# Kernel optimization log

Hardware: AMD Instinct MI355X
Metric: run time of the kernel (lower is better)

The kernel has to match this reference:

```python
import jax, jax.numpy as jnp
import numpy as np

B, IN_DIM, HID = 4096, 1024, 1024


def _linear(x, W, b):
    # torch nn.Linear: y = x @ W.T + b, W is [out, in]
    return x @ W.T + b


def setup_inputs() -> dict:
    key = jax.random.key(0)
    ks = jax.random.split(key, 15)
    s_in = 1.0 / np.sqrt(IN_DIM + HID)
    s_x = 1.0 / np.sqrt(IN_DIM)
    s_h = 1.0 / np.sqrt(HID)
    return {
        "x": jax.random.normal(ks[0], (B, IN_DIM), jnp.float32),
        "h_prev": jax.random.normal(ks[1], (B, HID), jnp.float32),
        "c_prev": jax.random.normal(ks[2], (B, HID), jnp.float32),
        "Wi": jax.random.normal(ks[3], (HID, IN_DIM + HID), jnp.float32) * s_in,
        "bi": jax.random.normal(ks[4], (HID,), jnp.float32) * s_in,
        "Wf": jax.random.normal(ks[5], (HID, IN_DIM + HID), jnp.float32) * s_in,
        "bf": jax.random.normal(ks[6], (HID,), jnp.float32) * s_in,
        "Wo": jax.random.normal(ks[7], (HID, IN_DIM + HID), jnp.float32) * s_in,
        "bo": jax.random.normal(ks[8], (HID,), jnp.float32) * s_in,
        "Wxs": jax.random.normal(ks[9], (HID, IN_DIM), jnp.float32) * s_x,
        "bxs": jax.random.normal(ks[10], (HID,), jnp.float32) * s_x,
        "Wxg": jax.random.normal(ks[11], (HID, IN_DIM), jnp.float32) * s_x,
        "bxg": jax.random.normal(ks[12], (HID,), jnp.float32) * s_x,
        "Whg": jax.random.normal(ks[13], (HID, HID), jnp.float32) * s_h,
        "bhg": jax.random.normal(ks[14], (HID,), jnp.float32) * s_h,
    }


def reference(x, h_prev, c_prev, Wi, bi, Wf, bf, Wo, bo, Wxs, bxs, Wxg, bxg, Whg, bhg):
    # Fuse the three (in_dim+hid)->hid gate GEMMs into one concatenated GEMM.
    concat = jnp.concatenate([x, h_prev], axis=-1)          # [B, in_dim+hid]
    W_ifo = jnp.concatenate([Wi, Wf, Wo], axis=0)           # [3*hid, in_dim+hid]
    b_ifo = jnp.concatenate([bi, bf, bo], axis=0)           # [3*hid]
    gates = jax.nn.sigmoid(_linear(concat, W_ifo, b_ifo))   # [B, 3*hid]
    i_t, f_t, o_t = jnp.split(gates, 3, axis=-1)
    s_t = _linear(x, Wxs, bxs)
    cand_lin = _linear(x, Wxg, bxg) + _linear(h_prev, Whg, bhg)
    g_t = jnp.tanh(s_t * cand_lin)
    # refined=False branch
    c_t = f_t * c_prev + i_t * g_t
    h_t = o_t * jnp.tanh(c_t)
    return (h_t, c_t)
```

## Files before the change

kernel.cpp:

```cpp
#include <hip/hip_runtime.h>

typedef unsigned short u16;
typedef __attribute__((ext_vector_type(8))) __bf16 bf16x8;
typedef __attribute__((ext_vector_type(4))) float f32x4;
typedef __attribute__((ext_vector_type(4))) unsigned short u16x4;

#define AS1 __attribute__((address_space(1)))
#define AS3 __attribute__((address_space(3)))

#define OB_X    0L
#define OB_H    4194304L
#define OB_WI   8388608L
#define OB_WF   10485760L
#define OB_WO   12582912L
#define OB_WXS  14680064L
#define OB_WXG  15728640L
#define OB_WHG  16777216L
#define BLOB_EL 17825792L
#define BLOB_BYTES (BLOB_EL * 2)

__device__ __forceinline__ float b2f(u16 u) {
    return __uint_as_float(((unsigned)u) << 16);
}
__device__ __forceinline__ u16 f2b(float f) {
    unsigned u = __float_as_uint(f);
    u += 0x7fffu + ((u >> 16) & 1u);
    return (u16)(u >> 16);
}
__device__ __forceinline__ f32x4 loadY4(const u16* p) {
    u16x4 v = *(const u16x4*)p;
    f32x4 r;
    r.x = b2f(v.x); r.y = b2f(v.y); r.z = b2f(v.z); r.w = b2f(v.w);
    return r;
}

__global__ __launch_bounds__(256) void convert_all(
    const float* __restrict__ x, const float* __restrict__ h,
    const float* __restrict__ Wi, const float* __restrict__ Wf,
    const float* __restrict__ Wo, const float* __restrict__ Wxs,
    const float* __restrict__ Wxg, const float* __restrict__ Whg,
    u16* __restrict__ blob)
{
    long e = ((long)blockIdx.x * 256 + threadIdx.x) * 8;
    const float* src; long off;
    if      (e < OB_H)   { src = x;   off = e; }
    else if (e < OB_WI)  { src = h;   off = e - OB_H; }
    else if (e < OB_WF)  { src = Wi;  off = e - OB_WI; }
    else if (e < OB_WO)  { src = Wf;  off = e - OB_WF; }
    else if (e < OB_WXS) { src = Wo;  off = e - OB_WO; }
    else if (e < OB_WXG) { src = Wxs; off = e - OB_WXS; }
    else if (e < OB_WHG) { src = Wxg; off = e - OB_WXG; }
    else                 { src = Whg; off = e - OB_WHG; }
    f32x4 v0 = *(const f32x4*)(src + off);
    f32x4 v1 = *(const f32x4*)(src + off + 4);
    u16x4 o0, o1;
    o0.x = f2b(v0.x); o0.y = f2b(v0.y); o0.z = f2b(v0.z); o0.w = f2b(v0.w);
    o1.x = f2b(v1.x); o1.y = f2b(v1.y); o1.z = f2b(v1.z); o1.w = f2b(v1.w);
    *(u16x4*)(blob + e) = o0;
    *(u16x4*)(blob + e + 4) = o1;
}

__global__ __launch_bounds__(256, 3) void srulstm_gemm(
    const u16* __restrict__ blob, u16* __restrict__ Y)
{
    __shared__ __align__(16) u16 As[128 * 64];
    __shared__ __align__(16) u16 Bs[128 * 64];

    const u16* x   = blob + OB_X;
    const u16* h   = blob + OB_H;
    const u16* Wi  = blob + OB_WI;
    const u16* Wf  = blob + OB_WF;
    const u16* Wo  = blob + OB_WO;
    const u16* Wxs = blob + OB_WXS;
    const u16* Wxg = blob + OB_WXG;
    const u16* Whg = blob + OB_WHG;

    const int t = threadIdx.x;
    const int n0 = blockIdx.x * 128;
    const int m0 = blockIdx.y * 128;
    const int seg = n0 >> 10;
    const int row0 = n0 & 1023;

    const u16* bLo; const u16* bHi; int bLd; int kLim;
    if (seg == 0)      { bLo = Wi  + row0 * 2048; bHi = bLo + 1024;        bLd = 2048; kLim = 2048; }
    else if (seg == 1) { bLo = Wf  + row0 * 2048; bHi = bLo + 1024;        bLd = 2048; kLim = 2048; }
    else if (seg == 2) { bLo = Wo  + row0 * 2048; bHi = bLo + 1024;        bLd = 2048; kLim = 2048; }
    else if (seg == 3) { bLo = Wxg + row0 * 1024; bHi = Whg + row0 * 1024; bLd = 1024; kLim = 2048; }
    else               { bLo = Wxs + row0 * 1024; bHi = bLo;               bLd = 1024; kLim = 1024; }

    const u16* aLo = x + m0 * 1024;
    const u16* aHi = h + m0 * 1024;

    const int lane = t & 63;
    const int wave = t >> 6;
    const int wm = (wave >> 1) << 6;
    const int wn = (wave & 1) << 6;
    const int fr = lane & 15;
    const int fq = lane >> 4;
    const int r7 = fr & 7;

    f32x4 acc[4][4] = {};

    const int er = t >> 3;
    const int gsw = (((t & 7) ^ (er & 7)) << 3);

    for (int k0 = 0; k0 < kLim; k0 += 64) {
        const int kc = k0 & 1023;
        const u16* aSrc = ((k0 < 1024) ? aLo : aHi) + kc;
        const u16* bSrc = ((k0 < 1024) ? bLo : bHi) + kc;
#pragma unroll
        for (int it = 0; it < 4; ++it) {
            const int row = it * 32 + er;
            __builtin_amdgcn_global_load_lds(
                (AS1 void*)(aSrc + row * 1024 + gsw),
                (AS3 void*)(As + (it * 256 + t) * 8), 16, 0, 0);
        }
#pragma unroll
        for (int it = 0; it < 4; ++it) {
            const int row = it * 32 + er;
            __builtin_amdgcn_global_load_lds(
                (AS1 void*)(bSrc + row * bLd + gsw),
                (AS3 void*)(Bs + (it * 256 + t) * 8), 16, 0, 0);
        }
        __syncthreads();
#pragma unroll
        for (int kk = 0; kk < 64; kk += 32) {
            const int sw = ((((kk >> 3) + fq) ^ r7) << 3);
            bf16x8 a[4], b[4];
#pragma unroll
            for (int mi = 0; mi < 4; ++mi)
                a[mi] = *(const bf16x8*)(As + (wm + mi * 16 + fr) * 64 + sw);
#pragma unroll
            for (int ni = 0; ni < 4; ++ni)
                b[ni] = *(const bf16x8*)(Bs + (wn + ni * 16 + fr) * 64 + sw);
#pragma unroll
            for (int mi = 0; mi < 4; ++mi)
#pragma unroll
                for (int ni = 0; ni < 4; ++ni)
                    acc[mi][ni] = __builtin_amdgcn_mfma_f32_16x16x32_bf16(
                        a[mi], b[ni], acc[mi][ni], 0, 0, 0);
        }
        __syncthreads();
    }

    const int orow = m0 + wm + (fq << 2);
    const int ocol = n0 + wn + fr;
#pragma unroll
    for (int mi = 0; mi < 4; ++mi)
#pragma unroll
        for (int ni = 0; ni < 4; ++ni) {
            u16* yp = Y + (long)(orow + mi * 16) * 5120 + (ocol + ni * 16);
#pragma unroll
            for (int r = 0; r < 4; ++r)
                yp[(long)r * 5120] = f2b(acc[mi][ni][r]);
        }
}

__global__ __launch_bounds__(256) void srulstm_epilogue(
    const u16* __restrict__ Y, const float* __restrict__ c_prev,
    const float* __restrict__ bi, const float* __restrict__ bfv,
    const float* __restrict__ bo, const float* __restrict__ bxs,
    const float* __restrict__ bxg, const float* __restrict__ bhg,
    float* __restrict__ out)
{
    const int gid = blockIdx.x * 256 + threadIdx.x;
    const int b = gid >> 8;
    const int j = (gid & 255) << 2;
    const long yb = (long)b * 5120 + j;

    f32x4 zi = loadY4(Y + yb);
    f32x4 zf = loadY4(Y + yb + 1024);
    f32x4 zo = loadY4(Y + yb + 2048);
    f32x4 zc = loadY4(Y + yb + 3072);
    f32x4 zs = loadY4(Y + yb + 4096);

    f32x4 cp  = *(const f32x4*)(c_prev + (long)b * 1024 + j);
    f32x4 vbi = *(const f32x4*)(bi + j);
    f32x4 vbf = *(const f32x4*)(bfv + j);
    f32x4 vbo = *(const f32x4*)(bo + j);
    f32x4 vbs = *(const f32x4*)(bxs + j);
    f32x4 vbg = *(const f32x4*)(bxg + j);
    f32x4 vbh = *(const f32x4*)(bhg + j);

    f32x4 ho, co;
#pragma unroll
    for (int r = 0; r < 4; ++r) {
        float i_t = 1.f / (1.f + __expf(-(zi[r] + vbi[r])));
        float f_t = 1.f / (1.f + __expf(-(zf[r] + vbf[r])));
        float o_t = 1.f / (1.f + __expf(-(zo[r] + vbo[r])));
        float s_t = zs[r] + vbs[r];
        float cand = zc[r] + vbg[r] + vbh[r];
        float g_t = tanhf(s_t * cand);
        float c_t = f_t * cp[r] + i_t * g_t;
        float h_t = o_t * tanhf(c_t);
        ho[r] = h_t;
        co[r] = c_t;
    }
    *(f32x4*)(out + (long)b * 1024 + j) = ho;
    *(f32x4*)(out + 4194304L + (long)b * 1024 + j) = co;
}

extern "C" void kernel_launch(void* const* d_in, const int* in_sizes, int n_in,
                              void* d_out, int out_size, void* d_ws, size_t ws_size,
                              hipStream_t stream)
{
    u16* blob = (u16*)d_ws;
    u16* Y = blob + BLOB_EL;
    float* out = (float*)d_out;

    dim3 gg(40, 32), gb(256);
    dim3 eg(4096), eb(256);
    const long convBlocks = BLOB_EL / 8 / 256;

    convert_all<<<dim3(convBlocks), dim3(256), 0, stream>>>(
        (const float*)d_in[0], (const float*)d_in[1], (const float*)d_in[3],
        (const float*)d_in[5], (const float*)d_in[7], (const float*)d_in[9],
        (const float*)d_in[11], (const float*)d_in[13], blob);

    srulstm_gemm<<<gg, gb, 0, stream>>>(blob, Y);

    srulstm_epilogue<<<eg, eb, 0, stream>>>(
        Y, (const float*)d_in[2], (const float*)d_in[4], (const float*)d_in[6],
        (const float*)d_in[8], (const float*)d_in[10], (const float*)d_in[12],
        (const float*)d_in[14], out);
}
```

Before: 248.5 us.

## Fuse all gate GEMMs and LSTM epilogue into one kernel per hidden tile

Each block now computes all five gate pre-activations (i, f, o, candidate, s) for a 64-column hidden slice and 128 batch rows, sharing one staged A tile across five B tiles. The LSTM elementwise epilogue runs directly on the accumulators, which removes the bf16 intermediate Y buffer and the separate epilogue launch. This trades higher register pressure (160 accumulator VGPRs, occupancy hint lowered to 2) and fewer, larger blocks (512 vs 1280). It also uses scalar, partially coalesced epilogue loads and stores in place of vector ones.

```diff
diff --git a/kernel.cpp b/kernel.cpp
--- a/kernel.cpp
+++ b/kernel.cpp
@@ -17,21 +17,11 @@
 #define OB_WXG  15728640L
 #define OB_WHG  16777216L
 #define BLOB_EL 17825792L
-#define BLOB_BYTES (BLOB_EL * 2)
-
-__device__ __forceinline__ float b2f(u16 u) {
-    return __uint_as_float(((unsigned)u) << 16);
-}
+
 __device__ __forceinline__ u16 f2b(float f) {
     unsigned u = __float_as_uint(f);
     u += 0x7fffu + ((u >> 16) & 1u);
     return (u16)(u >> 16);
-}
-__device__ __forceinline__ f32x4 loadY4(const u16* p) {
-    u16x4 v = *(const u16x4*)p;
-    f32x4 r;
-    r.x = b2f(v.x); r.y = b2f(v.y); r.z = b2f(v.z); r.w = b2f(v.w);
-    return r;
 }
 
 __global__ __launch_bounds__(256) void convert_all(
@@ -60,33 +50,45 @@
     *(u16x4*)(blob + e + 4) = o1;
 }
 
-__global__ __launch_bounds__(256, 3) void srulstm_gemm(
-    const u16* __restrict__ blob, u16* __restrict__ Y)
+__device__ __forceinline__ void stageB(u16* dst, const u16* src, int ld,
+                                       int t, int er, int gsw) {
+#pragma unroll
+    for (int it = 0; it < 2; ++it) {
+        const int row = it * 32 + er;
+        __builtin_amdgcn_global_load_lds(
+            (AS1 void*)(src + row * ld + gsw),
+            (AS3 void*)(dst + (it * 256 + t) * 8), 16, 0, 0);
+    }
+}
+
+__device__ __forceinline__ float sigf(float z) {
+    return 1.f / (1.f + __expf(-z));
+}
+
+__global__ __launch_bounds__(256, 2) void srulstm_fused(
+    const u16* __restrict__ blob,
+    const float* __restrict__ c_prev,
+    const float* __restrict__ bi, const float* __restrict__ bfv,
+    const float* __restrict__ bo, const float* __restrict__ bxs,
+    const float* __restrict__ bxg, const float* __restrict__ bhg,
+    float* __restrict__ out)
 {
     __shared__ __align__(16) u16 As[128 * 64];
-    __shared__ __align__(16) u16 Bs[128 * 64];
+    __shared__ __align__(16) u16 Bs[5 * 64 * 64];
 
     const u16* x   = blob + OB_X;
     const u16* h   = blob + OB_H;
-    const u16* Wi  = blob + OB_WI;
-    const u16* Wf  = blob + OB_WF;
-    const u16* Wo  = blob + OB_WO;
-    const u16* Wxs = blob + OB_WXS;
-    const u16* Wxg = blob + OB_WXG;
-    const u16* Whg = blob + OB_WHG;
 
     const int t = threadIdx.x;
-    const int n0 = blockIdx.x * 128;
+    const int j0 = blockIdx.x * 64;
     const int m0 = blockIdx.y * 128;
-    const int seg = n0 >> 10;
-    const int row0 = n0 & 1023;
-
-    const u16* bLo; const u16* bHi; int bLd; int kLim;
-    if (seg == 0)      { bLo = Wi  + row0 * 2048; bHi = bLo + 1024;        bLd = 2048; kLim = 2048; }
-    else if (seg == 1) { bLo = Wf  + row0 * 2048; bHi = bLo + 1024;        bLd = 2048; kLim = 2048; }
-    else if (seg == 2) { bLo = Wo  + row0 * 2048; bHi = bLo + 1024;        bLd = 2048; kLim = 2048; }
-    else if (seg == 3) { bLo = Wxg + row0 * 1024; bHi = Whg + row0 * 1024; bLd = 1024; kLim = 2048; }
-    else               { bLo = Wxs + row0 * 1024; bHi = bLo;               bLd = 1024; kLim = 1024; }
+
+    const u16* w0   = blob + OB_WI  + j0 * 2048;
+    const u16* w1   = blob + OB_WF  + j0 * 2048;
+    const u16* w2   = blob + OB_WO  + j0 * 2048;
+    const u16* w3lo = blob + OB_WXG + j0 * 1024;
+    const u16* w3hi = blob + OB_WHG + j0 * 1024;
+    const u16* w4   = blob + OB_WXS + j0 * 1024;
 
     const u16* aLo = x + m0 * 1024;
     const u16* aHi = h + m0 * 1024;
@@ -94,20 +96,18 @@
     const int lane = t & 63;
     const int wave = t >> 6;
     const int wm = (wave >> 1) << 6;
-    const int wn = (wave & 1) << 6;
+    const int wn = (wave & 1) << 5;
     const int fr = lane & 15;
     const int fq = lane >> 4;
     const int r7 = fr & 7;
 
-    f32x4 acc[4][4] = {};
+    f32x4 acc[5][4][2] = {};
 
     const int er = t >> 3;
     const int gsw = (((t & 7) ^ (er & 7)) << 3);
 
-    for (int k0 = 0; k0 < kLim; k0 += 64) {
-        const int kc = k0 & 1023;
-        const u16* aSrc = ((k0 < 1024) ? aLo : aHi) + kc;
-        const u16* bSrc = ((k0 < 1024) ? bLo : bHi) + kc;
+    for (int k0 = 0; k0 < 2048; k0 += 64) {
+        const u16* aSrc = ((k0 < 1024) ? aLo : aHi) + (k0 & 1023);
 #pragma unroll
         for (int it = 0; it < 4; ++it) {
             const int row = it * 32 + er;
@@ -115,89 +115,74 @@
                 (AS1 void*)(aSrc + row * 1024 + gsw),
                 (AS3 void*)(As + (it * 256 + t) * 8), 16, 0, 0);
         }
-#pragma unroll
-        for (int it = 0; it < 4; ++it) {
-            const int row = it * 32 + er;
-            __builtin_amdgcn_global_load_lds(
-                (AS1 void*)(bSrc + row * bLd + gsw),
-                (AS3 void*)(Bs + (it * 256 + t) * 8), 16, 0, 0);
-        }
+        stageB(Bs,         w0 + k0, 2048, t, er, gsw);
+        stageB(Bs + 4096,  w1 + k0, 2048, t, er, gsw);
+        stageB(Bs + 8192,  w2 + k0, 2048, t, er, gsw);
+        stageB(Bs + 12288, (k0 < 1024) ? (w3lo + k0) : (w3hi + (k0 - 1024)),
+               1024, t, er, gsw);
+        if (k0 < 1024)
+            stageB(Bs + 16384, w4 + k0, 1024, t, er, gsw);
         __syncthreads();
 #pragma unroll
         for (int kk = 0; kk < 64; kk += 32) {
             const int sw = ((((kk >> 3) + fq) ^ r7) << 3);
-            bf16x8 a[4], b[4];
+            bf16x8 a[4];
 #pragma unroll
             for (int mi = 0; mi < 4; ++mi)
                 a[mi] = *(const bf16x8*)(As + (wm + mi * 16 + fr) * 64 + sw);
 #pragma unroll
-            for (int ni = 0; ni < 4; ++ni)
-                b[ni] = *(const bf16x8*)(Bs + (wn + ni * 16 + fr) * 64 + sw);
-#pragma unroll
-            for (int mi = 0; mi < 4; ++mi)
-#pragma unroll
-                for (int ni = 0; ni < 4; ++ni)
-                    acc[mi][ni] = __builtin_amdgcn_mfma_f32_16x16x32_bf16(
-                        a[mi], b[ni], acc[mi][ni], 0, 0, 0);
+            for (int s = 0; s < 4; ++s) {
+                bf16x8 b0 = *(const bf16x8*)(Bs + s * 4096 + (wn + fr) * 64 + sw);
+                bf16x8 b1 = *(const bf16x8*)(Bs + s * 4096 + (wn + 16 + fr) * 64 + sw);
+#pragma unroll
+                for (int mi = 0; mi < 4; ++mi) {
+                    acc[s][mi][0] = __builtin_amdgcn_mfma_f32_16x16x32_bf16(
+                        a[mi], b0, acc[s][mi][0], 0, 0, 0);
+                    acc[s][mi][1] = __builtin_amdgcn_mfma_f32_16x16x32_bf16(
+                        a[mi], b1, acc[s][mi][1], 0, 0, 0);
+                }
+            }
+            if (k0 < 1024) {
+                bf16x8 b0 = *(const bf16x8*)(Bs + 16384 + (wn + fr) * 64 + sw);
+                bf16x8 b1 = *(const bf16x8*)(Bs + 16384 + (wn + 16 + fr) * 64 + sw);
+#pragma unroll
+                for (int mi = 0; mi < 4; ++mi) {
+                    acc[4][mi][0] = __builtin_amdgcn_mfma_f32_16x16x32_bf16(
+                        a[mi], b0, acc[4][mi][0], 0, 0, 0);
+                    acc[4][mi][1] = __builtin_amdgcn_mfma_f32_16x16x32_bf16(
+                        a[mi], b1, acc[4][mi][1], 0, 0, 0);
+                }
+            }
         }
         __syncthreads();
     }
 
     const int orow = m0 + wm + (fq << 2);
-    const int ocol = n0 + wn + fr;
-#pragma unroll
-    for (int mi = 0; mi < 4; ++mi)
-#pragma unroll
-        for (int ni = 0; ni < 4; ++ni) {
-            u16* yp = Y + (long)(orow + mi * 16) * 5120 + (ocol + ni * 16);
-#pragma unroll
-            for (int r = 0; r < 4; ++r)
-                yp[(long)r * 5120] = f2b(acc[mi][ni][r]);
+    const int ocol = j0 + wn + fr;
+#pragma unroll
+    for (int ni = 0; ni < 2; ++ni) {
+        const int col = ocol + ni * 16;
+        const float bi_v = bi[col],  bf_v = bfv[col], bo_v = bo[col];
+        const float bs_v = bxs[col], bg_v = bxg[col], bh_v = bhg[col];
+#pragma unroll
+        for (int mi = 0; mi < 4; ++mi) {
+#pragma unroll
+            for (int r = 0; r < 4; ++r) {
+                const long idx = (long)(orow + mi * 16 + r) * 1024 + col;
+                const float cp = c_prev[idx];
+                const float i_t = sigf(acc[0][mi][ni][r] + bi_v);
+                const float f_t = sigf(acc[1][mi][ni][r] + bf_v);
+                const float o_t = sigf(acc[2][mi][ni][r] + bo_v);
+                const float cand = acc[3][mi][ni][r] + bg_v + bh_v;
+                const float s_t  = acc[4][mi][ni][r] + bs_v;
+                const float g_t = tanhf(s_t * cand);
+                const float c_t = f_t * cp + i_t * g_t;
+                const float h_t = o_t * tanhf(c_t);
+                out[idx] = h_t;
+                out[4194304L + idx] = c_t;
+            }
         }
-}
-
-__global__ __launch_bounds__(256) void srulstm_epilogue(
-    const u16* __restrict__ Y, const float* __restrict__ c_prev,
-    const float* __restrict__ bi, const float* __restrict__ bfv,
-    const float* __restrict__ bo, const float* __restrict__ bxs,
-    const float* __restrict__ bxg, const float* __restrict__ bhg,
-    float* __restrict__ out)
-{
-    const int gid = blockIdx.x * 256 + threadIdx.x;
-    const int b = gid >> 8;
-    const int j = (gid & 255) << 2;
-    const long yb = (long)b * 5120 + j;
-
-    f32x4 zi = loadY4(Y + yb);
-    f32x4 zf = loadY4(Y + yb + 1024);
-    f32x4 zo = loadY4(Y + yb + 2048);
-    f32x4 zc = loadY4(Y + yb + 3072);
-    f32x4 zs = loadY4(Y + yb + 4096);
-
-    f32x4 cp  = *(const f32x4*)(c_prev + (long)b * 1024 + j);
-    f32x4 vbi = *(const f32x4*)(bi + j);
-    f32x4 vbf = *(const f32x4*)(bfv + j);
-    f32x4 vbo = *(const f32x4*)(bo + j);
-    f32x4 vbs = *(const f32x4*)(bxs + j);
-    f32x4 vbg = *(const f32x4*)(bxg + j);
-    f32x4 vbh = *(const f32x4*)(bhg + j);
-
-    f32x4 ho, co;
-#pragma unroll
-    for (int r = 0; r < 4; ++r) {
-        float i_t = 1.f / (1.f + __expf(-(zi[r] + vbi[r])));
-        float f_t = 1.f / (1.f + __expf(-(zf[r] + vbf[r])));
-        float o_t = 1.f / (1.f + __expf(-(zo[r] + vbo[r])));
-        float s_t = zs[r] + vbs[r];
-        float cand = zc[r] + vbg[r] + vbh[r];
-        float g_t = tanhf(s_t * cand);
-        float c_t = f_t * cp[r] + i_t * g_t;
-        float h_t = o_t * tanhf(c_t);
-        ho[r] = h_t;
-        co[r] = c_t;
     }
-    *(f32x4*)(out + (long)b * 1024 + j) = ho;
-    *(f32x4*)(out + 4194304L + (long)b * 1024 + j) = co;
 }
 
 extern "C" void kernel_launch(void* const* d_in, const int* in_sizes, int n_in,
@@ -205,11 +190,8 @@
                               hipStream_t stream)
 {
     u16* blob = (u16*)d_ws;
-    u16* Y = blob + BLOB_EL;
     float* out = (float*)d_out;
 
-    dim3 gg(40, 32), gb(256);
-    dim3 eg(4096), eb(256);
     const long convBlocks = BLOB_EL / 8 / 256;
 
     convert_all<<<dim3(convBlocks), dim3(256), 0, stream>>>(
@@ -217,10 +199,8 @@
         (const float*)d_in[5], (const float*)d_in[7], (const float*)d_in[9],
         (const float*)d_in[11], (const float*)d_in[13], blob);
 
-    srulstm_gemm<<<gg, gb, 0, stream>>>(blob, Y);
-
-    srulstm_epilogue<<<eg, eb, 0, stream>>>(
-        Y, (const float*)d_in[2], (const float*)d_in[4], (const float*)d_in[6],
+    srulstm_fused<<<dim3(16, 32), dim3(256), 0, stream>>>(
+        blob, (const float*)d_in[2], (const float*)d_in[4], (const float*)d_in[6],
         (const float*)d_in[8], (const float*)d_in[10], (const float*)d_in[12],
         (const float*)d_in[14], out);
 }
```

Measured after the change: 227.3 us. 1.09x faster.
